# Kernel tuning notes

Hardware: AMD Instinct MI355X
Metric: run time of the kernel (lower is better)

The kernel has to match this reference:

```python
import jax, jax.numpy as jnp
import numpy as np

EPS = 1e-6
BANDWIDTH = 10


def _norm_last(x):
    return x / jnp.sum(x, axis=-1, keepdims=True)


def _causal_linear_branch(Q, K, V, eps):
    # Q,K: [N,L,H,E] feature-mapped; V: [N,L,H,D]
    Q = _norm_last(Q)
    K = _norm_last(K)
    Kcum = jnp.cumsum(K, axis=1)                                   # [N,L,H,E]
    Z = 1.0 / (jnp.einsum('nlhe,nlhe->nlh', Q, Kcum) + eps)        # [N,L,H]
    # causal_dot_product: running sum of outer products K_s V_s^T
    S = jnp.cumsum(K[..., :, None] * V[..., None, :], axis=1)       # [N,L,H,E,D]
    Vn = jnp.einsum('nlhe,nlhed->nlhd', Q, S)                       # [N,L,H,D]
    return Vn * Z[..., None]


def setup_inputs() -> dict:
    key = jax.random.key(0)
    k1, k2, k3, k4 = jax.random.split(key, 4)
    N, L, H, E = 2, 2048, 8, 32
    return {
        'queries': jax.random.normal(k1, (N, L, H, E), dtype=jnp.float32),
        'keys': jax.random.normal(k2, (N, L, H, E), dtype=jnp.float32),
        'values': jax.random.normal(k3, (N, L, H, E), dtype=jnp.float32),
        'key_lengths': jnp.ones((N, L), dtype=jnp.float32),
        'W1': 0.02 * jax.random.normal(k4, (1, 1, H, E), dtype=jnp.float32),
        'W2': jnp.ones((1, 1, H, E), dtype=jnp.float32) * 0.5,
        'W3': jnp.ones((1, 1, H, E), dtype=jnp.float32) * 0.5,
    }


def reference(queries, keys, values, key_lengths, W1, W2, W3):
    klen = key_lengths[:, :, None, None]
    # kernel 1: elu feature map phi(x) = elu(x) + 1
    Q1 = jax.nn.elu(queries) + 1.0
    K1 = (jax.nn.elu(keys) + 1.0) * klen
    LV = W2 * _causal_linear_branch(Q1, K1, values, EPS)
    # kernel 2: squared elu feature map phi(x) = (elu(x) + 1)^2
    Q2 = (jax.nn.elu(queries) + 1.0) ** 2
    K2 = ((jax.nn.elu(keys) + 1.0) ** 2) * klen
    LV = LV + W3 * _causal_linear_branch(Q2, K2, values, EPS)
    # sparse near-field: banded causal softmax attention
    N, L, H, E = queries.shape
    temp = 1.0 / np.sqrt(E).astype(np.float32)
    QK = jnp.einsum('nlhe,nshe->nhls', queries * temp, keys)       # [N,H,L,S]
    li = jnp.arange(L)[:, None]
    si = jnp.arange(L)[None, :]
    band = (si <= li) & (si > li - BANDWIDTH)                      # keep band of width `bandwidth`
    QK = jnp.where(band[None, None], QK, -jnp.inf)
    A = jax.nn.softmax(QK, axis=-1)                                # dropout is identity (p=0 / eval)
    SV = jnp.einsum('nhls,nshd->nlhd', A, values)
    return W1 * SV + LV
```

## Files before the change

### kernel.cpp

```cpp
#include <hip/hip_runtime.h>
#include <cmath>

constexpr int NN = 2;
constexpr int LL = 2048;
constexpr int HH = 8;
constexpr int EE = 32;
constexpr int CC = 32;
constexpr int NCH = LL / CC;
constexpr int NB  = NN * HH * NCH;
constexpr int BWD = 10;
constexpr int REC  = 2 * (EE * EE + EE);
constexpr int R16  = REC * 2 / 16;
constexpr int OFF_S1 = 0, OFF_K1 = 1024, OFF_S2 = 1056, OFF_K2 = 2080;
constexpr int SK = EE + 4;
constexpr int SB = 40;

using f32x16 = __attribute__((ext_vector_type(16))) float;
using s16x8  = __attribute__((ext_vector_type(8)))  short;

__device__ __forceinline__ float elu1(float x) {
    return x > 0.f ? x + 1.f : __expf(x);
}
__device__ __forceinline__ unsigned short bfr(float x) {
    union { float f; unsigned u; } v; v.f = x;
    return (unsigned short)((v.u + 0x7FFFu + ((v.u >> 16) & 1u)) >> 16);
}
__device__ __forceinline__ float bf2f(unsigned short b) {
    union { unsigned u; float f; } v; v.u = ((unsigned)b) << 16;
    return v.f;
}

__global__ __launch_bounds__(256) void chunksum_kernel(
    const float* __restrict__ Kin, const float* __restrict__ Vin,
    unsigned short* __restrict__ ws)
{
    __shared__ __align__(16) unsigned short K1T[EE][SB];
    __shared__ __align__(16) unsigned short K2T[EE][SB];
    __shared__ __align__(16) unsigned short VT [EE][SB];

    const int b  = blockIdx.x;
    const int c  = b & (NCH - 1);
    const int nh = b >> 6;
    const int t  = threadIdx.x;
    const int lane = t & 31;
    const int grp  = t >> 5;

    for (int r = grp; r < CC; r += 8) {
        const int l = c * CC + r;
        const int base = ((nh >> 3) * LL + l) * HH * EE + (nh & 7) * EE + lane;
        const float k = Kin[base];
        const float v = Vin[base];
        const float f1 = elu1(k);
        const float f2 = f1 * f1;
        float s1 = f1, s2 = f2;
        #pragma unroll
        for (int m = 1; m < 32; m <<= 1) {
            s1 += __shfl_xor(s1, m, 32);
            s2 += __shfl_xor(s2, m, 32);
        }
        K1T[lane][r] = bfr(f1 * __builtin_amdgcn_rcpf(s1));
        K2T[lane][r] = bfr(f2 * __builtin_amdgcn_rcpf(s2));
        VT [lane][r] = bfr(v);
    }
    __syncthreads();

    const int wid = t >> 6;
    const int l64 = t & 63;
    const int l31 = l64 & 31;
    const int hi5 = l64 >> 5;

    if (wid < 2) {
        const unsigned short* KT = wid ? &K2T[0][0] : &K1T[0][0];
        const s16x8 va0 = *(const s16x8*)&VT[l31][8 * hi5];
        const s16x8 va1 = *(const s16x8*)&VT[l31][16 + 8 * hi5];
        const s16x8 kb0 = *(const s16x8*)&KT[l31 * SB + 8 * hi5];
        const s16x8 kb1 = *(const s16x8*)&KT[l31 * SB + 16 + 8 * hi5];
        s16x8 ones;
        #pragma unroll
        for (int i = 0; i < 8; ++i) ones[i] = (short)0x3F80;

        f32x16 S = {};
        S = __builtin_amdgcn_mfma_f32_32x32x16_bf16(va0, kb0, S, 0, 0, 0);
        S = __builtin_amdgcn_mfma_f32_32x32x16_bf16(va1, kb1, S, 0, 0, 0);
        f32x16 Dk = {};
        Dk = __builtin_amdgcn_mfma_f32_32x32x16_bf16(ones, kb0, Dk, 0, 0, 0);
        Dk = __builtin_amdgcn_mfma_f32_32x32x16_bf16(ones, kb1, Dk, 0, 0, 0);

        unsigned short* wb = ws + (size_t)b * REC + (wid ? OFF_S2 : OFF_S1);
        unsigned short* wk = ws + (size_t)b * REC + (wid ? OFF_K2 : OFF_K1);
        #pragma unroll
        for (int k = 0; k < 16; ++k) {
            const int row = (k & 3) + 8 * (k >> 2) + 4 * hi5;
            wb[row * EE + l31] = bfr(S[k]);
        }
        if (hi5 == 0) wk[l31] = bfr(Dk[0]);
    }
}

__global__ __launch_bounds__(192) void prefix_kernel(unsigned short* __restrict__ ws)
{
    const int g = blockIdx.x / 11;
    const int e = (blockIdx.x % 11) * 192 + threadIdx.x;
    unsigned short* base = ws + (size_t)g * NCH * REC + e;
    float run = 0.f;
    {
        unsigned short v[32];
        #pragma unroll
        for (int c = 0; c < 32; ++c) v[c] = base[(size_t)c * REC];
        #pragma unroll
        for (int c = 0; c < 32; ++c) {
            base[(size_t)c * REC] = bfr(run);
            run += bf2f(v[c]);
        }
    }
    {
        unsigned short v[32];
        #pragma unroll
        for (int c = 0; c < 32; ++c) v[c] = base[(size_t)(32 + c) * REC];
        #pragma unroll
        for (int c = 0; c < 32; ++c) {
            base[(size_t)(32 + c) * REC] = bfr(run);
            run += bf2f(v[c]);
        }
    }
}

__global__ __launch_bounds__(256) void fused_kernel(
    const float* __restrict__ Qin, const float* __restrict__ Kin,
    const float* __restrict__ Vin,
    const float* __restrict__ W1, const float* __restrict__ W2,
    const float* __restrict__ W3, const unsigned short* __restrict__ ws,
    float* __restrict__ out)
{
    __shared__ float Vs [CC + 9][SK];
    __shared__ __align__(16) unsigned short Qfb[CC][SB];
    __shared__ __align__(16) unsigned short Kfb[CC][SB];
    __shared__ __align__(16) unsigned short Vtb[EE][SB];
    __shared__ __align__(16) unsigned short Pb1[CC][SB];
    __shared__ __align__(16) unsigned short Pb2[CC][SB];
    __shared__ float Ob1[CC][SK];
    __shared__ float Ob2[CC][SK];
    __shared__ __align__(16) union {
        float kr[(CC + 9) * SK];
        unsigned short sp[REC];
    } U;

    const int b  = blockIdx.x;
    const int c  = b & (NCH - 1);
    const int nh = b >> 6;
    const int h  = nh & 7;
    const int n  = nh >> 3;
    const int l0 = c * CC;
    const int t  = threadIdx.x;
    const int lane = t & 31;
    const int grp  = t >> 5;

    const uint4* wbv = (const uint4*)(ws + (size_t)b * REC);
    const uint4 s0 = wbv[t];
    uint4 s1 = {0u, 0u, 0u, 0u};
    if (t < R16 - 256) s1 = wbv[256 + t];

    for (int r = grp; r < CC; r += 8) {
        const int l = l0 + r;
        const int base = ((n * LL + l) * HH + h) * EE + lane;
        const float k = Kin[base];
        const float v = Vin[base];
        const float q = Qin[base];
        Kfb[r][lane] = bfr(elu1(k));
        Qfb[r][lane] = bfr(elu1(q));
        Vs[9 + r][lane] = v;
        Vtb[lane][r] = bfr(v);
        U.kr[(9 + r) * SK + lane] = k;
    }
    for (int idx = t; idx < 9 * 32; idx += 256) {
        const int rr = idx >> 5, ln = idx & 31;
        const int l = l0 - 9 + rr;
        float kv = 0.f, vv = 0.f;
        if (l >= 0) {
            const int gbase = ((n * LL + l) * HH + h) * EE + ln;
            kv = Kin[gbase];
            vv = Vin[gbase];
        }
        U.kr[rr * SK + ln] = kv;
        Vs[rr][ln] = vv;
    }

    const int r   = t >> 3;
    const int sub = t & 7;
    const int d0  = sub * 4;
    const int l   = l0 + r;

    const float4 q4 = *(const float4*)&Qin[((n * LL + l) * HH + h) * EE + d0];
    __syncthreads();

    float bnd[4];
    {
        const float temp = 0.17677669529663687f;
        float mx = -INFINITY, den = 0.f;
        float sv0 = 0.f, sv1 = 0.f, sv2 = 0.f, sv3 = 0.f;
        #pragma unroll
        for (int jj = 0; jj < BWD; ++jj) {
            const int j = l - (BWD - 1) + jj;
            if (j >= 0) {
                const float4 k4 = *(const float4*)&U.kr[(r + jj) * SK + d0];
                float p = q4.x*k4.x + q4.y*k4.y + q4.z*k4.z + q4.w*k4.w;
                p += __shfl_xor(p, 1, 8); p += __shfl_xor(p, 2, 8); p += __shfl_xor(p, 4, 8);
                const float s  = p * temp;
                const float mn = fmaxf(mx, s);
                const float c1 = __expf(mx - mn);
                const float c2 = __expf(s - mn);
                const float4 v4 = *(const float4*)&Vs[r + jj][d0];
                den = den * c1 + c2;
                sv0 = sv0 * c1 + c2 * v4.x;
                sv1 = sv1 * c1 + c2 * v4.y;
                sv2 = sv2 * c1 + c2 * v4.z;
                sv3 = sv3 * c1 + c2 * v4.w;
                mx = mn;
            }
        }
        const float inv = 1.f / den;
        const float4 w1 = *(const float4*)&W1[h * EE + d0];
        bnd[0] = w1.x * sv0 * inv; bnd[1] = w1.y * sv1 * inv;
        bnd[2] = w1.z * sv2 * inv; bnd[3] = w1.w * sv3 * inv;
    }
    __syncthreads();

    ((uint4*)U.sp)[t] = s0;
    if (t < R16 - 256) ((uint4*)U.sp)[256 + t] = s1;
    __syncthreads();

    const int wid = t >> 6;
    const int l64 = t & 63;
    const int l31 = l64 & 31;
    const int hi5 = l64 >> 5;

    if ((wid & 1) == 0) {
        const bool b2 = (wid == 2);
        const unsigned short* Spt = U.sp + (b2 ? OFF_S2 : OFF_S1);
        const unsigned short* kp  = U.sp + (b2 ? OFF_K2 : OFF_K1);
        const float* Wv = b2 ? W3 : W2;
        unsigned short* Pb = b2 ? &Pb2[0][0] : &Pb1[0][0];
        float* Ob = b2 ? &Ob2[0][0] : &Ob1[0][0];

        s16x8 qa0 = *(const s16x8*)&Qfb[l31][8 * hi5];
        s16x8 qa1 = *(const s16x8*)&Qfb[l31][16 + 8 * hi5];
        s16x8 kb0 = *(const s16x8*)&Kfb[l31][8 * hi5];
        s16x8 kb1 = *(const s16x8*)&Kfb[l31][16 + 8 * hi5];
        if (b2) {
            #pragma unroll
            for (int i = 0; i < 8; ++i) {
                float f;
                f = bf2f((unsigned short)qa0[i]); qa0[i] = (short)bfr(f * f);
                f = bf2f((unsigned short)qa1[i]); qa1[i] = (short)bfr(f * f);
                f = bf2f((unsigned short)kb0[i]); kb0[i] = (short)bfr(f * f);
                f = bf2f((unsigned short)kb1[i]); kb1[i] = (short)bfr(f * f);
            }
        }
        s16x8 ones;
        #pragma unroll
        for (int i = 0; i < 8; ++i) ones[i] = (short)0x3F80;

        f32x16 Dk = {};
        Dk = __builtin_amdgcn_mfma_f32_32x32x16_bf16(ones, kb0, Dk, 0, 0, 0);
        Dk = __builtin_amdgcn_mfma_f32_32x32x16_bf16(ones, kb1, Dk, 0, 0, 0);
        f32x16 P = {};
        P = __builtin_amdgcn_mfma_f32_32x32x16_bf16(qa0, kb0, P, 0, 0, 0);
        P = __builtin_amdgcn_mfma_f32_32x32x16_bf16(qa1, kb1, P, 0, 0, 0);

        const float ki = __builtin_amdgcn_rcpf(Dk[0]);
        #pragma unroll
        for (int k = 0; k < 16; ++k) {
            const int row = (k & 3) + 8 * (k >> 2) + 4 * hi5;
            Pb[row * SB + l31] = bfr((l31 <= row) ? P[k] * ki : 0.f);
        }
        const s16x8 pa0 = *(const s16x8*)&Pb[l31 * SB + 8 * hi5];
        const s16x8 pa1 = *(const s16x8*)&Pb[l31 * SB + 16 + 8 * hi5];

        const s16x8 vb0 = *(const s16x8*)&Vtb[l31][8 * hi5];
        const s16x8 vb1 = *(const s16x8*)&Vtb[l31][16 + 8 * hi5];
        const s16x8 sb0 = *(const s16x8*)&Spt[l31 * EE + 8 * hi5];
        const s16x8 sb1 = *(const s16x8*)&Spt[l31 * EE + 16 + 8 * hi5];
        const s16x8 rb0 = *(const s16x8*)&kp[8 * hi5];
        const s16x8 rb1 = *(const s16x8*)&kp[16 + 8 * hi5];

        f32x16 A = {};
        A = __builtin_amdgcn_mfma_f32_32x32x16_bf16(pa0, vb0, A, 0, 0, 0);
        A = __builtin_amdgcn_mfma_f32_32x32x16_bf16(pa1, vb1, A, 0, 0, 0);
        A = __builtin_amdgcn_mfma_f32_32x32x16_bf16(qa0, sb0, A, 0, 0, 0);
        A = __builtin_amdgcn_mfma_f32_32x32x16_bf16(qa1, sb1, A, 0, 0, 0);

        f32x16 Dp = {};
        Dp = __builtin_amdgcn_mfma_f32_32x32x16_bf16(pa0, ones, Dp, 0, 0, 0);
        Dp = __builtin_amdgcn_mfma_f32_32x32x16_bf16(pa1, ones, Dp, 0, 0, 0);
        Dp = __builtin_amdgcn_mfma_f32_32x32x16_bf16(qa0, rb0, Dp, 0, 0, 0);
        Dp = __builtin_amdgcn_mfma_f32_32x32x16_bf16(qa1, rb1, Dp, 0, 0, 0);

        const float wv = Wv[h * EE + l31];
        #pragma unroll
        for (int k = 0; k < 16; ++k) {
            const int row = (k & 3) + 8 * (k >> 2) + 4 * hi5;
            Ob[row * SK + l31] = wv * A[k] * __builtin_amdgcn_rcpf(Dp[k]);
        }
    }
    __syncthreads();

    const float4 o1 = *(const float4*)&Ob1[r][d0];
    const float4 o2 = *(const float4*)&Ob2[r][d0];
    float4 o;
    o.x = bnd[0] + o1.x + o2.x;
    o.y = bnd[1] + o1.y + o2.y;
    o.z = bnd[2] + o1.z + o2.z;
    o.w = bnd[3] + o1.w + o2.w;
    *(float4*)&out[((n * LL + l) * HH + h) * EE + d0] = o;
}

extern "C" void kernel_launch(void* const* d_in, const int* in_sizes, int n_in,
                              void* d_out, int out_size, void* d_ws, size_t ws_size,
                              hipStream_t stream)
{
    (void)in_sizes; (void)n_in; (void)out_size; (void)ws_size;
    const float* Q  = (const float*)d_in[0];
    const float* K  = (const float*)d_in[1];
    const float* V  = (const float*)d_in[2];
    const float* W1 = (const float*)d_in[4];
    const float* W2 = (const float*)d_in[5];
    const float* W3 = (const float*)d_in[6];
    float* out = (float*)d_out;
    unsigned short* ws = (unsigned short*)d_ws;

    chunksum_kernel<<<NB,           256, 0, stream>>>(K, V, ws);
    prefix_kernel  <<<NN * HH * 11, 192, 0, stream>>>(ws);
    fused_kernel   <<<NB,           256, 0, stream>>>(Q, K, V, W1, W2, W3, ws, out);
}
```

Before: 90.14 us.

## Move banded softmax attention onto idle wavefront using bf16 MFMA

The scalar per-thread banded softmax, with its shuffles and online rescaling, is replaced by MFMA tiles run on wavefront 1, which was idle while wavefronts 0 and 2 ran the linear branches. Q·K scores for the 41-row key window come from two 32x32 MFMAs, are masked to the band, go through softmax, and are multiplied by V with three more MFMAs. This removes one synchronization phase and the fp32 shared-memory staging of K and V. In exchange, banded attention now uses bf16 inputs, probabilities and output, which lowers accuracy and adds some wasted masked MFMA work.

```diff
diff --git a/kernel.cpp b/kernel.cpp
--- a/kernel.cpp
+++ b/kernel.cpp
@@ -14,6 +14,7 @@
 constexpr int OFF_S1 = 0, OFF_K1 = 1024, OFF_S2 = 1056, OFF_K2 = 2080;
 constexpr int SK = EE + 4;
 constexpr int SB = 40;
+constexpr int VS = 48;
 
 using f32x16 = __attribute__((ext_vector_type(16))) float;
 using s16x8  = __attribute__((ext_vector_type(8)))  short;
@@ -132,18 +133,18 @@
     const float* __restrict__ W3, const unsigned short* __restrict__ ws,
     float* __restrict__ out)
 {
-    __shared__ float Vs [CC + 9][SK];
     __shared__ __align__(16) unsigned short Qfb[CC][SB];
     __shared__ __align__(16) unsigned short Kfb[CC][SB];
-    __shared__ __align__(16) unsigned short Vtb[EE][SB];
+    __shared__ __align__(16) unsigned short Qrb[CC][SB];
+    __shared__ __align__(16) unsigned short Krb[41][SB];
+    __shared__ __align__(16) unsigned short Vtb[EE][VS];
     __shared__ __align__(16) unsigned short Pb1[CC][SB];
     __shared__ __align__(16) unsigned short Pb2[CC][SB];
+    __shared__ __align__(16) unsigned short Pbd[CC][VS];
+    __shared__ __align__(16) unsigned short Obb[CC][SB];
     __shared__ float Ob1[CC][SK];
     __shared__ float Ob2[CC][SK];
-    __shared__ __align__(16) union {
-        float kr[(CC + 9) * SK];
-        unsigned short sp[REC];
-    } U;
+    __shared__ __align__(16) unsigned short sp[REC];
 
     const int b  = blockIdx.x;
     const int c  = b & (NCH - 1);
@@ -160,6 +161,7 @@
     uint4 s1 = {0u, 0u, 0u, 0u};
     if (t < R16 - 256) s1 = wbv[256 + t];
 
+    const float temp = 0.17677669529663687f;
     for (int r = grp; r < CC; r += 8) {
         const int l = l0 + r;
         const int base = ((n * LL + l) * HH + h) * EE + lane;
@@ -168,9 +170,9 @@
         const float q = Qin[base];
         Kfb[r][lane] = bfr(elu1(k));
         Qfb[r][lane] = bfr(elu1(q));
-        Vs[9 + r][lane] = v;
+        Qrb[r][lane] = bfr(q * temp);
+        Krb[9 + r][lane] = bfr(k);
         Vtb[lane][r] = bfr(v);
-        U.kr[(9 + r) * SK + lane] = k;
     }
     for (int idx = t; idx < 9 * 32; idx += 256) {
         const int rr = idx >> 5, ln = idx & 31;
@@ -181,52 +183,15 @@
             kv = Kin[gbase];
             vv = Vin[gbase];
         }
-        U.kr[rr * SK + ln] = kv;
-        Vs[rr][ln] = vv;
-    }
-
-    const int r   = t >> 3;
-    const int sub = t & 7;
-    const int d0  = sub * 4;
-    const int l   = l0 + r;
-
-    const float4 q4 = *(const float4*)&Qin[((n * LL + l) * HH + h) * EE + d0];
-    __syncthreads();
-
-    float bnd[4];
-    {
-        const float temp = 0.17677669529663687f;
-        float mx = -INFINITY, den = 0.f;
-        float sv0 = 0.f, sv1 = 0.f, sv2 = 0.f, sv3 = 0.f;
-        #pragma unroll
-        for (int jj = 0; jj < BWD; ++jj) {
-            const int j = l - (BWD - 1) + jj;
-            if (j >= 0) {
-                const float4 k4 = *(const float4*)&U.kr[(r + jj) * SK + d0];
-                float p = q4.x*k4.x + q4.y*k4.y + q4.z*k4.z + q4.w*k4.w;
-                p += __shfl_xor(p, 1, 8); p += __shfl_xor(p, 2, 8); p += __shfl_xor(p, 4, 8);
-                const float s  = p * temp;
-                const float mn = fmaxf(mx, s);
-                const float c1 = __expf(mx - mn);
-                const float c2 = __expf(s - mn);
-                const float4 v4 = *(const float4*)&Vs[r + jj][d0];
-                den = den * c1 + c2;
-                sv0 = sv0 * c1 + c2 * v4.x;
-                sv1 = sv1 * c1 + c2 * v4.y;
-                sv2 = sv2 * c1 + c2 * v4.z;
-                sv3 = sv3 * c1 + c2 * v4.w;
-                mx = mn;
-            }
-        }
-        const float inv = 1.f / den;
-        const float4 w1 = *(const float4*)&W1[h * EE + d0];
-        bnd[0] = w1.x * sv0 * inv; bnd[1] = w1.y * sv1 * inv;
-        bnd[2] = w1.z * sv2 * inv; bnd[3] = w1.w * sv3 * inv;
-    }
-    __syncthreads();
-
-    ((uint4*)U.sp)[t] = s0;
-    if (t < R16 - 256) ((uint4*)U.sp)[256 + t] = s1;
+        Krb[rr][ln] = bfr(kv);
+        Vtb[ln][32 + rr] = bfr(vv);
+    }
+    if (t < 32) {
+        #pragma unroll
+        for (int cc = 41; cc < 48; ++cc) Vtb[t][cc] = 0;
+    }
+    ((uint4*)sp)[t] = s0;
+    if (t < R16 - 256) ((uint4*)sp)[256 + t] = s1;
     __syncthreads();
 
     const int wid = t >> 6;
@@ -236,8 +201,8 @@
 
     if ((wid & 1) == 0) {
         const bool b2 = (wid == 2);
-        const unsigned short* Spt = U.sp + (b2 ? OFF_S2 : OFF_S1);
-        const unsigned short* kp  = U.sp + (b2 ? OFF_K2 : OFF_K1);
+        const unsigned short* Spt = sp + (b2 ? OFF_S2 : OFF_S1);
+        const unsigned short* kp  = sp + (b2 ? OFF_K2 : OFF_K1);
         const float* Wv = b2 ? W3 : W2;
         unsigned short* Pb = b2 ? &Pb2[0][0] : &Pb1[0][0];
         float* Ob = b2 ? &Ob2[0][0] : &Ob1[0][0];
@@ -301,16 +266,92 @@
             const int row = (k & 3) + 8 * (k >> 2) + 4 * hi5;
             Ob[row * SK + l31] = wv * A[k] * __builtin_amdgcn_rcpf(Dp[k]);
         }
+    } else if (wid == 1) {
+        const int q = l31;
+        const int jmin = (l0 >= 9) ? 0 : 9 - l0;
+        const s16x8 qb0 = *(const s16x8*)&Qrb[q][8 * hi5];
+        const s16x8 qb1 = *(const s16x8*)&Qrb[q][16 + 8 * hi5];
+        const s16x8 kl0 = *(const s16x8*)&Krb[l31][8 * hi5];
+        const s16x8 kl1 = *(const s16x8*)&Krb[l31][16 + 8 * hi5];
+        const s16x8 kh0 = *(const s16x8*)&Krb[9 + l31][8 * hi5];
+        const s16x8 kh1 = *(const s16x8*)&Krb[9 + l31][16 + 8 * hi5];
+
+        f32x16 Slo = {}, Shi = {};
+        Slo = __builtin_amdgcn_mfma_f32_32x32x16_bf16(kl0, qb0, Slo, 0, 0, 0);
+        Slo = __builtin_amdgcn_mfma_f32_32x32x16_bf16(kl1, qb1, Slo, 0, 0, 0);
+        Shi = __builtin_amdgcn_mfma_f32_32x32x16_bf16(kh0, qb0, Shi, 0, 0, 0);
+        Shi = __builtin_amdgcn_mfma_f32_32x32x16_bf16(kh1, qb1, Shi, 0, 0, 0);
+
+        float m = -INFINITY;
+        #pragma unroll
+        for (int k = 0; k < 16; ++k) {
+            const int jl = (k & 3) + 8 * (k >> 2) + 4 * hi5;
+            const int jh = jl + 9;
+            if (jl <= 8 && jl >= q && jl >= jmin) m = fmaxf(m, Slo[k]);
+            if (jh >= q && jh <= q + 9) m = fmaxf(m, Shi[k]);
+        }
+        m = fmaxf(m, __shfl_xor(m, 32, 64));
+        float den = 0.f;
+        float plo[16], phi[16];
+        #pragma unroll
+        for (int k = 0; k < 16; ++k) {
+            const int jl = (k & 3) + 8 * (k >> 2) + 4 * hi5;
+            const int jh = jl + 9;
+            plo[k] = __expf(Slo[k] - m);
+            phi[k] = __expf(Shi[k] - m);
+            if (jl <= 8 && jl >= q && jl >= jmin) den += plo[k];
+            if (jh >= q && jh <= q + 9) den += phi[k];
+        }
+        den += __shfl_xor(den, 32, 64);
+        const float inv = __builtin_amdgcn_rcpf(den);
+
+        {
+            const uint4 z = {0u, 0u, 0u, 0u};
+            *(uint4*)&Pbd[q][24 * hi5 + 0]  = z;
+            *(uint4*)&Pbd[q][24 * hi5 + 8]  = z;
+            *(uint4*)&Pbd[q][24 * hi5 + 16] = z;
+        }
+        #pragma unroll
+        for (int k = 0; k < 16; ++k) {
+            const int jl = (k & 3) + 8 * (k >> 2) + 4 * hi5;
+            const int jh = jl + 9;
+            if (jl <= 8 && jl >= q && jl >= jmin)
+                Pbd[q][32 + jl] = bfr(plo[k] * inv);
+            if (jh >= q && jh <= q + 9)
+                Pbd[q][jh - 9] = bfr(phi[k] * inv);
+        }
+
+        const s16x8 pa0 = *(const s16x8*)&Pbd[l31][8 * hi5];
+        const s16x8 pa1 = *(const s16x8*)&Pbd[l31][16 + 8 * hi5];
+        const s16x8 pa2 = *(const s16x8*)&Pbd[l31][32 + 8 * hi5];
+        const s16x8 vb0 = *(const s16x8*)&Vtb[l31][8 * hi5];
+        const s16x8 vb1 = *(const s16x8*)&Vtb[l31][16 + 8 * hi5];
+        const s16x8 vb2 = *(const s16x8*)&Vtb[l31][32 + 8 * hi5];
+        f32x16 OB = {};
+        OB = __builtin_amdgcn_mfma_f32_32x32x16_bf16(pa0, vb0, OB, 0, 0, 0);
+        OB = __builtin_amdgcn_mfma_f32_32x32x16_bf16(pa1, vb1, OB, 0, 0, 0);
+        OB = __builtin_amdgcn_mfma_f32_32x32x16_bf16(pa2, vb2, OB, 0, 0, 0);
+
+        const float w1v = W1[h * EE + l31];
+        #pragma unroll
+        for (int k = 0; k < 16; ++k) {
+            const int row = (k & 3) + 8 * (k >> 2) + 4 * hi5;
+            Obb[row][l31] = bfr(w1v * OB[k]);
+        }
     }
     __syncthreads();
 
+    const int r   = t >> 3;
+    const int d0  = (t & 7) * 4;
+    const int l   = l0 + r;
     const float4 o1 = *(const float4*)&Ob1[r][d0];
     const float4 o2 = *(const float4*)&Ob2[r][d0];
+    const ushort4 ob = *(const ushort4*)&Obb[r][d0];
     float4 o;
-    o.x = bnd[0] + o1.x + o2.x;
-    o.y = bnd[1] + o1.y + o2.y;
-    o.z = bnd[2] + o1.z + o2.z;
-    o.w = bnd[3] + o1.w + o2.w;
+    o.x = bf2f(ob.x) + o1.x + o2.x;
+    o.y = bf2f(ob.y) + o1.y + o2.y;
+    o.z = bf2f(ob.z) + o1.z + o2.z;
+    o.w = bf2f(ob.w) + o1.w + o2.w;
     *(float4*)&out[((n * LL + l) * HH + h) * EE + d0] = o;
 }
 
```

New measurement: 87.72 us. 2.7% less time.
